# Kernel tuning notes

Hardware: AMD Instinct MI355X
Metric: run time of the kernel (lower is better)

## Reference

```python
import jax, jax.numpy as jnp
import numpy as np

B, T, C = 2, 2048, 1024
H, DK, DV = 16, 64, 64


def setup_inputs() -> dict:
    key = jax.random.key(0)
    ks = jax.random.split(key, 12)
    p = lambda k, shape: (jax.random.normal(k, shape, dtype=jnp.float32) * 0.02)
    Q = jax.random.normal(ks[0], (B, T, C), dtype=jnp.float32)
    K = jax.random.normal(ks[1], (B, T, C), dtype=jnp.float32)
    V = jax.random.normal(ks[2], (B, T, C), dtype=jnp.float32)
    Wq, bq = p(ks[3], (C, H * DK)), p(ks[4], (H * DK,))
    Wk, bk = p(ks[5], (C, H * DK)), p(ks[6], (H * DK,))
    Wv, bv = p(ks[7], (C, H * DV)), p(ks[8], (H * DV,))
    Wo, bo = p(ks[9], (H * DV, C)), p(ks[10], (C,))
    # additive causal mask, broadcastable to (B, H, T, T)
    causal = jnp.tril(jnp.ones((T, T), dtype=bool))
    mask = jnp.where(causal, 0.0, -1e9).astype(jnp.float32)[None, None]
    return {"Q": Q, "K": K, "V": V, "Wq": Wq, "bq": bq, "Wk": Wk, "bk": bk,
            "Wv": Wv, "bv": bv, "Wo": Wo, "bo": bo, "mask": mask}


def reference(Q, K, V, Wq, bq, Wk, bk, Wv, bv, Wo, bo, mask):
    def split(x, d):  # (B,T,H*d) -> (B,H,T,d)
        return x.reshape(B, T, H, d).transpose(0, 2, 1, 3)

    q = split(Q @ Wq + bq, DK)
    k = split(K @ Wk + bk, DK)
    v = split(V @ Wv + bv, DV)
    # NOTE: faithful to source — mask added BEFORE scaling by 1/sqrt(dk)
    scores = (jnp.einsum('bhqd,bhkd->bhqk', q, k) + mask) / float(np.sqrt(DK))
    attn = jax.nn.softmax(scores, axis=-1)
    out = jnp.einsum('bhqk,bhkd->bhqd', attn, v)  # (B,H,T,DV)
    out = out.transpose(0, 2, 1, 3).reshape(B, T, H * DV)
    return out @ Wo + bo
```

## Files before the change

kernel.cpp:

```cpp
#include <hip/hip_runtime.h>
#include <cstdint>
#include <cstddef>

#define TB 2
#define TT 2048
#define TC 1024
#define TH 16
#define TD 64
#define MROWS (TB*TT)

typedef __attribute__((ext_vector_type(8))) short bf16x8;
typedef __attribute__((ext_vector_type(4))) float f32x4;

#define QSCL2 0.18033688011112042f
#define MASKL2 (-1.8033688e8f)

__device__ __forceinline__ unsigned short f2bf(float f) {
  union { float f; unsigned int u; } x; x.f = f;
  unsigned int r = x.u + 0x7fffu + ((x.u >> 16) & 1u);
  return (unsigned short)(r >> 16);
}

__device__ __forceinline__ void gload16(const void* g, void* l) {
  __builtin_amdgcn_global_load_lds((const __attribute__((address_space(1))) void*)g,
                                   (__attribute__((address_space(3))) void*)l, 16, 0, 0);
}

#define WAITVM(N) do { asm volatile("s_waitcnt vmcnt(" #N ")" ::: "memory"); \
                       __builtin_amdgcn_sched_barrier(0); } while (0)

__device__ __forceinline__ float exp2h(float x) {
  float r;
  asm("v_exp_f32 %0, %1" : "=v"(r) : "v"(x));
  return r;
}

__global__ __launch_bounds__(256) void prep_kernel(
    const float* __restrict__ W0, const float* __restrict__ W1,
    const float* __restrict__ W2, const float* __restrict__ W3,
    unsigned short* __restrict__ T0, unsigned short* __restrict__ T1,
    unsigned short* __restrict__ T2, unsigned short* __restrict__ T3,
    const float* __restrict__ Q, const float* __restrict__ K, const float* __restrict__ V,
    unsigned short* __restrict__ qc, unsigned short* __restrict__ kc,
    unsigned short* __restrict__ vc) {
  const int z = blockIdx.z;
  if (z < 4) {
    const float* W = z == 0 ? W0 : (z == 1 ? W1 : (z == 2 ? W2 : W3));
    unsigned short* WT = z == 0 ? T0 : (z == 1 ? T1 : (z == 2 ? T2 : T3));
    __shared__ float ts[32][33];
    int tx = threadIdx.x & 31, ty = threadIdx.x >> 5;
    int n0 = blockIdx.x * 32, k0 = blockIdx.y * 32;
#pragma unroll
    for (int r = 0; r < 32; r += 8)
      ts[ty + r][tx] = W[(size_t)(k0 + ty + r) * TC + n0 + tx];
    __syncthreads();
#pragma unroll
    for (int r = 0; r < 32; r += 8)
      WT[(size_t)(n0 + ty + r) * TC + k0 + tx] = f2bf(ts[tx][ty + r]);
  } else {
    const int zt = z - 4;
    const float* in = zt == 0 ? Q : (zt == 1 ? K : V);
    unsigned short* out = zt == 0 ? qc : (zt == 1 ? kc : vc);
    const int lb = blockIdx.y * 32 + blockIdx.x;
#pragma unroll
    for (int c = 0; c < 2; ++c) {
      int i = lb * 4096 + c * 2048 + threadIdx.x * 8;
      float4 f0 = *(const float4*)(in + i);
      float4 f1 = *(const float4*)(in + i + 4);
      union { unsigned short u[8]; int4 v; } pk;
      pk.u[0] = f2bf(f0.x); pk.u[1] = f2bf(f0.y); pk.u[2] = f2bf(f0.z); pk.u[3] = f2bf(f0.w);
      pk.u[4] = f2bf(f1.x); pk.u[5] = f2bf(f1.y); pk.u[6] = f2bf(f1.z); pk.u[7] = f2bf(f1.w);
      *(int4*)(out + i) = pk.v;
    }
  }
}

__global__ __launch_bounds__(256) void wtrans4_kernel(
    const float* __restrict__ W0, const float* __restrict__ W1,
    const float* __restrict__ W2, const float* __restrict__ W3,
    unsigned short* __restrict__ T0, unsigned short* __restrict__ T1,
    unsigned short* __restrict__ T2, unsigned short* __restrict__ T3) {
  const int z = blockIdx.z;
  const float* W = z == 0 ? W0 : (z == 1 ? W1 : (z == 2 ? W2 : W3));
  unsigned short* WT = z == 0 ? T0 : (z == 1 ? T1 : (z == 2 ? T2 : T3));
  __shared__ float ts[32][33];
  int tx = threadIdx.x & 31, ty = threadIdx.x >> 5;
  int n0 = blockIdx.x * 32, k0 = blockIdx.y * 32;
#pragma unroll
  for (int r = 0; r < 32; r += 8)
    ts[ty + r][tx] = W[(size_t)(k0 + ty + r) * TC + n0 + tx];
  __syncthreads();
#pragma unroll
  for (int r = 0; r < 32; r += 8)
    WT[(size_t)(n0 + ty + r) * TC + k0 + tx] = f2bf(ts[tx][ty + r]);
}

__global__ __launch_bounds__(256) void cast3_kernel(
    const float* __restrict__ A, const float* __restrict__ B, const float* __restrict__ C,
    unsigned short* __restrict__ oa, unsigned short* __restrict__ ob,
    unsigned short* __restrict__ oc) {
  const int z = blockIdx.y;
  const float* in = z == 0 ? A : (z == 1 ? B : C);
  unsigned short* out = z == 0 ? oa : (z == 1 ? ob : oc);
  int i = (blockIdx.x * 256 + threadIdx.x) * 8;
  float4 f0 = *(const float4*)(in + i);
  float4 f1 = *(const float4*)(in + i + 4);
  union { unsigned short u[8]; int4 v; } pk;
  pk.u[0] = f2bf(f0.x); pk.u[1] = f2bf(f0.y); pk.u[2] = f2bf(f0.z); pk.u[3] = f2bf(f0.w);
  pk.u[4] = f2bf(f1.x); pk.u[5] = f2bf(f1.y); pk.u[6] = f2bf(f1.z); pk.u[7] = f2bf(f1.w);
  *(int4*)(out + i) = pk.v;
}

__global__ __launch_bounds__(256, 6)
void qkv_gemm_kernel(const unsigned short* __restrict__ Aq, const unsigned short* __restrict__ Ak,
                     const unsigned short* __restrict__ Av,
                     const unsigned short* __restrict__ BTq, const unsigned short* __restrict__ BTk,
                     const unsigned short* __restrict__ BTv,
                     const float* __restrict__ bq, const float* __restrict__ bk,
                     const float* __restrict__ bv,
                     unsigned short* __restrict__ Oq, unsigned short* __restrict__ Ok,
                     unsigned short* __restrict__ Ov, int zbase) {
  __shared__ __attribute__((aligned(16))) unsigned short As[128][64];
  __shared__ __attribute__((aligned(16))) unsigned short Bs[64][64];
  const int z = blockIdx.z + zbase;
  const unsigned short* A  = z == 0 ? Aq  : (z == 1 ? Ak  : Av);
  const unsigned short* Bt = z == 0 ? BTq : (z == 1 ? BTk : BTv);
  const float* bias        = z == 0 ? bq  : (z == 1 ? bk  : bv);
  unsigned short* Out      = z == 0 ? Oq  : (z == 1 ? Ok  : Ov);

  const int lin = blockIdx.y * 16 + blockIdx.x;
  const int swz = (lin & 7) * 64 + (lin >> 3);
  const int m0 = (swz >> 4) * 128, n0 = (swz & 15) * 64;

  const int tid = threadIdx.x, wave = tid >> 6, lane = tid & 63;
  const int lh = lane & 15, lq = lane >> 4;
  const int wr = wave >> 1, wc = wave & 1;
  const int srow = lane >> 3, sseg = (lane & 7) ^ srow;
  const f32x4 vzero = {0.f, 0.f, 0.f, 0.f};
  f32x4 acc[4][2];
#pragma unroll
  for (int i = 0; i < 4; ++i)
#pragma unroll
    for (int j = 0; j < 2; ++j) acc[i][j] = vzero;

  for (int k0 = 0; k0 < TC; k0 += 64) {
    __syncthreads();
#pragma unroll
    for (int c = 0; c < 4; ++c) {
      const int chunk = wave * 4 + c;
      const int row = chunk * 8 + srow;
      gload16(A + (size_t)(m0 + row) * TC + k0 + sseg * 8, &As[chunk * 8][0]);
    }
#pragma unroll
    for (int c = 0; c < 2; ++c) {
      const int chunk = wave * 2 + c;
      const int row = chunk * 8 + srow;
      gload16(Bt + (size_t)(n0 + row) * TC + k0 + sseg * 8, &Bs[chunk * 8][0]);
    }
    __syncthreads();
#pragma unroll
    for (int kk = 0; kk < 2; ++kk) {
      const int seg = kk * 4 + lq;
      bf16x8 a[4], b[2];
#pragma unroll
      for (int i = 0; i < 4; ++i) {
        int row = wr * 64 + i * 16 + lh;
        a[i] = *(const bf16x8*)&As[row][(seg ^ (row & 7)) << 3];
      }
#pragma unroll
      for (int j = 0; j < 2; ++j) {
        int row = wc * 32 + j * 16 + lh;
        b[j] = *(const bf16x8*)&Bs[row][(seg ^ (row & 7)) << 3];
      }
#pragma unroll
      for (int i = 0; i < 4; ++i)
#pragma unroll
        for (int j = 0; j < 2; ++j)
          acc[i][j] = __builtin_amdgcn_mfma_f32_16x16x32_bf16(a[i], b[j], acc[i][j], 0, 0, 0);
    }
  }

#pragma unroll
  for (int i = 0; i < 4; ++i)
#pragma unroll
    for (int j = 0; j < 2; ++j) {
      const int cg = n0 + wc * 32 + j * 16 + lh;
      const float bb = bias[cg];
      if (z == 2) {
        int rg0 = m0 + wr * 64 + i * 16 + lq * 4;
        int bidx = rg0 >> 11, t0 = rg0 & (TT - 1);
        int h = cg >> 6, d = cg & 63;
        unsigned long long pk = 0ull;
#pragma unroll
        for (int r = 0; r < 4; ++r)
          pk |= (unsigned long long)f2bf(acc[i][j][r] + bb) << (16 * r);
        *(unsigned long long*)(Out + ((size_t)((bidx * TH + h) * TD + d)) * TT + t0) = pk;
      } else {
#pragma unroll
        for (int r = 0; r < 4; ++r) {
          int rg = m0 + wr * 64 + i * 16 + lq * 4 + r;
          int bidx = rg >> 11, t = rg & (TT - 1);
          int h = cg >> 6, d = cg & 63;
          Out[((size_t)((bidx * TH + h) * TT + t)) * TD + d] = f2bf(acc[i][j][r] + bb);
        }
      }
    }
}

__global__ __launch_bounds__(256, 4)
void oproj_gemm_kernel(const unsigned short* __restrict__ A, const unsigned short* __restrict__ Bt,
                       const float* __restrict__ bias, float* __restrict__ Out) {
  __shared__ __attribute__((aligned(16))) unsigned short As[64][64];
  __shared__ __attribute__((aligned(16))) unsigned short Bs[64][64];
  const int lin = blockIdx.y * 16 + blockIdx.x;
  const int swz = (lin & 7) * 128 + (lin >> 3);
  const int m0 = (swz >> 4) * 64, n0 = (swz & 15) * 64;

  const int tid = threadIdx.x, wave = tid >> 6, lane = tid & 63;
  const int lh = lane & 15, lq = lane >> 4;
  const int wr = wave >> 1, wc = wave & 1;
  const int srow = lane >> 3, sseg = (lane & 7) ^ srow;
  const f32x4 vzero = {0.f, 0.f, 0.f, 0.f};
  f32x4 acc[2][2];
#pragma unroll
  for (int i = 0; i < 2; ++i)
#pragma unroll
    for (int j = 0; j < 2; ++j) acc[i][j] = vzero;

  for (int k0 = 0; k0 < TC; k0 += 64) {
    __syncthreads();
#pragma unroll
    for (int c = 0; c < 2; ++c) {
      const int chunk = wave * 2 + c;
      const int row = chunk * 8 + srow;
      gload16(A + (size_t)(m0 + row) * TC + k0 + sseg * 8, &As[chunk * 8][0]);
      gload16(Bt + (size_t)(n0 + row) * TC + k0 + sseg * 8, &Bs[chunk * 8][0]);
    }
    __syncthreads();
#pragma unroll
    for (int kk = 0; kk < 2; ++kk) {
      const int seg = kk * 4 + lq;
      bf16x8 a[2], b[2];
#pragma unroll
      for (int i = 0; i < 2; ++i) {
        int row = wr * 32 + i * 16 + lh;
        a[i] = *(const bf16x8*)&As[row][(seg ^ (row & 7)) << 3];
      }
#pragma unroll
      for (int j = 0; j < 2; ++j) {
        int row = wc * 32 + j * 16 + lh;
        b[j] = *(const bf16x8*)&Bs[row][(seg ^ (row & 7)) << 3];
      }
#pragma unroll
      for (int i = 0; i < 2; ++i)
#pragma unroll
        for (int j = 0; j < 2; ++j)
          acc[i][j] = __builtin_amdgcn_mfma_f32_16x16x32_bf16(a[i], b[j], acc[i][j], 0, 0, 0);
    }
  }

#pragma unroll
  for (int i = 0; i < 2; ++i)
#pragma unroll
    for (int j = 0; j < 2; ++j) {
      const int cg = n0 + wc * 32 + j * 16 + lh;
      const float bb = bias[cg];
#pragma unroll
      for (int r = 0; r < 4; ++r) {
        int rg = m0 + wr * 32 + i * 16 + lq * 4 + r;
        Out[(size_t)rg * TC + cg] = acc[i][j][r] + bb;
      }
    }
}

__global__ __launch_bounds__(256, 4)
void attn_kernel(const unsigned short* __restrict__ qb, const unsigned short* __restrict__ kb,
                 const unsigned short* __restrict__ vtb, unsigned short* __restrict__ ob) {
  __shared__ __attribute__((aligned(16))) unsigned short Qs[64][64];
  __shared__ __attribute__((aligned(16))) unsigned short Ks[2][64][64];
  __shared__ __attribute__((aligned(16))) unsigned short Vs[2][64][64];
  const int tid = threadIdx.x, wave = tid >> 6, lane = tid & 63;
  const int lh = lane & 15, lq = lane >> 4;
  const int srow = lane >> 3, sseg = (lane & 7) ^ srow;
  const int swzA = lh & 7;

  const int id = blockIdx.x;
  const int bh = (id & 7) * 4 + ((id >> 3) & 3);
  const int bx = 31 - (id >> 5);
  const size_t qkb = (size_t)bh * TT * TD;
  const size_t vob = (size_t)bh * TD * TT;
  const int bidx = bh >> 4, h = bh & 15;
  const f32x4 vzero = {0.f, 0.f, 0.f, 0.f};

  union { unsigned short u[8]; bf16x8 v; } onef;
#pragma unroll
  for (int i = 0; i < 8; ++i) onef.u[i] = 0x3F80;

  auto stageKV = [&](int buf, int t) {
    const int kv0 = t * 64;
#pragma unroll
    for (int c = 0; c < 2; ++c) {
      const int chunk = wave * 2 + c;
      const int row = chunk * 8 + srow;
      gload16(kb + qkb + (size_t)(kv0 + row) * TD + sseg * 8, &Ks[buf][chunk * 8][0]);
      gload16(vtb + vob + (size_t)row * TT + kv0 + sseg * 8, &Vs[buf][chunk * 8][0]);
    }
  };

  const int q0 = bx * 64;
  const int nt = bx + 1;
  const int q_g = q0 + wave * 16 + lh;

#pragma unroll
  for (int c = 0; c < 2; ++c) {
    const int chunk = wave * 2 + c;
    const int row = chunk * 8 + srow;
    gload16(qb + qkb + (size_t)(q0 + row) * TD + sseg * 8, &Qs[chunk * 8][0]);
  }
  stageKV(0, 0);
  WAITVM(0);
  bf16x8 aq[2];
  {
    const int row = wave * 16 + lh;
#pragma unroll
    for (int kk = 0; kk < 2; ++kk)
      aq[kk] = *(const bf16x8*)&Qs[row][((kk * 4 + lq) ^ (row & 7)) << 3];
  }
  f32x4 oacc[4], lacc = vzero;
#pragma unroll
  for (int jt = 0; jt < 4; ++jt) oacc[jt] = vzero;

  for (int t = 0; t < nt; ++t) {
    const int cur = t & 1;
    const int kv0 = t * 64;
    __builtin_amdgcn_s_barrier();
    if (t + 1 < nt) stageKV(cur ^ 1, t + 1);

    f32x4 accS[4];
#pragma unroll
    for (int j = 0; j < 4; ++j) accS[j] = vzero;
    __builtin_amdgcn_s_setprio(1);
#pragma unroll
    for (int kk = 0; kk < 2; ++kk) {
#pragma unroll
      for (int j = 0; j < 4; ++j) {
        bf16x8 bk = *(const bf16x8*)&Ks[cur][j * 16 + lh][((kk * 4 + lq) ^ swzA) << 3];
        accS[j] = __builtin_amdgcn_mfma_f32_16x16x32_bf16(bk, aq[kk], accS[j], 0, 0, 0);
      }
    }
    __builtin_amdgcn_s_setprio(0);

    float p_[16];
    if (t == bx) {
#pragma unroll
      for (int j = 0; j < 4; ++j)
#pragma unroll
        for (int r = 0; r < 4; ++r) {
          const int kvg = kv0 + j * 16 + lq * 4 + r;
          p_[j * 4 + r] = fmaf(accS[j][r], QSCL2, (kvg <= q_g) ? 0.f : MASKL2);
        }
    } else {
#pragma unroll
      for (int j = 0; j < 4; ++j)
#pragma unroll
        for (int r = 0; r < 4; ++r)
          p_[j * 4 + r] = accS[j][r] * QSCL2;
    }
#pragma unroll
    for (int i = 0; i < 16; ++i) p_[i] = exp2h(p_[i]);

    unsigned Dw[8];
#pragma unroll
    for (int j = 0; j < 4; ++j)
#pragma unroll
      for (int tt = 0; tt < 2; ++tt)
        asm("v_cvt_pk_bf16_f32 %0, %1, %2"
            : "=v"(Dw[j * 2 + tt]) : "v"(p_[j * 4 + 2 * tt]), "v"(p_[j * 4 + 2 * tt + 1]));
#pragma unroll
    for (int ks = 0; ks < 2; ++ks) {
      unsigned x0 = Dw[(2 * ks) * 2 + 0], y0 = Dw[(2 * ks + 1) * 2 + 0];
      unsigned x1 = Dw[(2 * ks) * 2 + 1], y1 = Dw[(2 * ks + 1) * 2 + 1];
      asm("v_permlane32_swap_b32 %0, %1" : "+v"(x0), "+v"(y0));
      asm("v_permlane16_swap_b32 %0, %1" : "+v"(x0), "+v"(y0));
      asm("v_permlane32_swap_b32 %0, %1" : "+v"(x1), "+v"(y1));
      asm("v_permlane16_swap_b32 %0, %1" : "+v"(x1), "+v"(y1));
      union { unsigned u[4]; bf16x8 v; } pb;
      pb.u[0] = x0; pb.u[1] = x1; pb.u[2] = y0; pb.u[3] = y1;
      __builtin_amdgcn_s_setprio(1);
#pragma unroll
      for (int jt = 0; jt < 4; ++jt) {
        bf16x8 av = *(const bf16x8*)&Vs[cur][jt * 16 + lh][((ks * 4 + lq) ^ swzA) << 3];
        oacc[jt] = __builtin_amdgcn_mfma_f32_16x16x32_bf16(av, pb.v, oacc[jt], 0, 0, 0);
      }
      lacc = __builtin_amdgcn_mfma_f32_16x16x32_bf16(onef.v, pb.v, lacc, 0, 0, 0);
      __builtin_amdgcn_s_setprio(0);
    }
    if (t + 1 < nt) WAITVM(0);
  }

  const float inv = 1.f / lacc[0];
  unsigned short* orow = ob + ((size_t)(bidx * TT + q_g)) * TC + h * TD;
#pragma unroll
  for (int jt = 0; jt < 4; ++jt) {
    unsigned long long pk = 0ull;
#pragma unroll
    for (int r = 0; r < 4; ++r)
      pk |= (unsigned long long)f2bf(oacc[jt][r] * inv) << (16 * r);
    *(unsigned long long*)(orow + jt * 16 + lq * 4) = pk;
  }
}

extern "C" void kernel_launch(void* const* d_in, const int* in_sizes, int n_in,
                              void* d_out, int out_size, void* d_ws, size_t ws_size,
                              hipStream_t stream) {
  const float* Q  = (const float*)d_in[0];
  const float* K  = (const float*)d_in[1];
  const float* V  = (const float*)d_in[2];
  const float* Wq = (const float*)d_in[3];
  const float* bq = (const float*)d_in[4];
  const float* Wk = (const float*)d_in[5];
  const float* bk = (const float*)d_in[6];
  const float* Wv = (const float*)d_in[7];
  const float* bv = (const float*)d_in[8];
  const float* Wo = (const float*)d_in[9];
  const float* bo = (const float*)d_in[10];
  float* out = (float*)d_out;

  char* ws = (char*)d_ws;
  const size_t MB = 1ull << 20;
  unsigned short* WqT = (unsigned short*)(ws + 0 * MB);
  unsigned short* WkT = (unsigned short*)(ws + 2 * MB);
  unsigned short* WvT = (unsigned short*)(ws + 4 * MB);
  unsigned short* WoT = (unsigned short*)(ws + 6 * MB);

  const bool fat = ws_size >= 56 * MB;
  unsigned short *qc, *kc, *vc, *qbuf, *kbuf, *vtbuf, *aout;
  if (fat) {
    qc    = (unsigned short*)(ws + 8 * MB);
    kc    = (unsigned short*)(ws + 16 * MB);
    vc    = (unsigned short*)(ws + 24 * MB);
    qbuf  = (unsigned short*)(ws + 32 * MB);
    kbuf  = (unsigned short*)(ws + 40 * MB);
    vtbuf = (unsigned short*)(ws + 48 * MB);
    aout  = qc;
  } else {
    qc = kc = vc = (unsigned short*)(ws + 8 * MB);
    qbuf  = (unsigned short*)(ws + 16 * MB);
    kbuf  = (unsigned short*)(ws + 24 * MB);
    vtbuf = (unsigned short*)(ws + 32 * MB);
    aout  = qc;
  }

  dim3 blk(256);
  if (fat) {
    prep_kernel<<<dim3(32, 32, 7), blk, 0, stream>>>(
        Wq, Wk, Wv, Wo, WqT, WkT, WvT, WoT, Q, K, V, qc, kc, vc);
    qkv_gemm_kernel<<<dim3(16, 32, 3), blk, 0, stream>>>(
        qc, kc, vc, WqT, WkT, WvT, bq, bk, bv, qbuf, kbuf, vtbuf, 0);
  } else {
    const int castGrid = MROWS * TC / (256 * 8);
    wtrans4_kernel<<<dim3(32, 32, 4), blk, 0, stream>>>(Wq, Wk, Wv, Wo, WqT, WkT, WvT, WoT);
    cast3_kernel<<<dim3(castGrid, 1), blk, 0, stream>>>(Q, Q, Q, qc, qc, qc);
    qkv_gemm_kernel<<<dim3(16, 32, 1), blk, 0, stream>>>(
        qc, qc, qc, WqT, WkT, WvT, bq, bk, bv, qbuf, kbuf, vtbuf, 0);
    cast3_kernel<<<dim3(castGrid, 1), blk, 0, stream>>>(K, K, K, kc, kc, kc);
    qkv_gemm_kernel<<<dim3(16, 32, 1), blk, 0, stream>>>(
        kc, kc, kc, WqT, WkT, WvT, bq, bk, bv, qbuf, kbuf, vtbuf, 1);
    cast3_kernel<<<dim3(castGrid, 1), blk, 0, stream>>>(V, V, V, vc, vc, vc);
    qkv_gemm_kernel<<<dim3(16, 32, 1), blk, 0, stream>>>(
        vc, vc, vc, WqT, WkT, WvT, bq, bk, bv, qbuf, kbuf, vtbuf, 2);
  }

  attn_kernel<<<dim3(1024), blk, 0, stream>>>(qbuf, kbuf, vtbuf, aout);

  oproj_gemm_kernel<<<dim3(16, 64), blk, 0, stream>>>(aout, WoT, bo, out);
}
```

Before: 102.8 us.

## Fuse fp32-to-bf16 activation cast into QKV GEMM and double-buffer output projection

Removes the separate activation cast pass: the QKV GEMM now reads fp32 Q/K/V directly, converts to bf16 with packed convert instructions and stores to LDS through registers instead of direct global-to-LDS loads. This drops a full write and re-read of the bf16 activation copies and the small-workspace fallback path. The output projection GEMM gains double-buffered LDS staging so the next K tile loads while the current tile is multiplied. The trade-off is that the QKV loads now pass through VGPRs and read twice as many bytes per tile, which may expose latency in the inner loop.

```diff
diff --git a/kernel.cpp b/kernel.cpp
--- a/kernel.cpp
+++ b/kernel.cpp
@@ -35,47 +35,13 @@
   return r;
 }
 
+__device__ __forceinline__ unsigned cvtpk(float lo, float hi) {
+  unsigned r;
+  asm("v_cvt_pk_bf16_f32 %0, %1, %2" : "=v"(r) : "v"(lo), "v"(hi));
+  return r;
+}
+
 __global__ __launch_bounds__(256) void prep_kernel(
-    const float* __restrict__ W0, const float* __restrict__ W1,
-    const float* __restrict__ W2, const float* __restrict__ W3,
-    unsigned short* __restrict__ T0, unsigned short* __restrict__ T1,
-    unsigned short* __restrict__ T2, unsigned short* __restrict__ T3,
-    const float* __restrict__ Q, const float* __restrict__ K, const float* __restrict__ V,
-    unsigned short* __restrict__ qc, unsigned short* __restrict__ kc,
-    unsigned short* __restrict__ vc) {
-  const int z = blockIdx.z;
-  if (z < 4) {
-    const float* W = z == 0 ? W0 : (z == 1 ? W1 : (z == 2 ? W2 : W3));
-    unsigned short* WT = z == 0 ? T0 : (z == 1 ? T1 : (z == 2 ? T2 : T3));
-    __shared__ float ts[32][33];
-    int tx = threadIdx.x & 31, ty = threadIdx.x >> 5;
-    int n0 = blockIdx.x * 32, k0 = blockIdx.y * 32;
-#pragma unroll
-    for (int r = 0; r < 32; r += 8)
-      ts[ty + r][tx] = W[(size_t)(k0 + ty + r) * TC + n0 + tx];
-    __syncthreads();
-#pragma unroll
-    for (int r = 0; r < 32; r += 8)
-      WT[(size_t)(n0 + ty + r) * TC + k0 + tx] = f2bf(ts[tx][ty + r]);
-  } else {
-    const int zt = z - 4;
-    const float* in = zt == 0 ? Q : (zt == 1 ? K : V);
-    unsigned short* out = zt == 0 ? qc : (zt == 1 ? kc : vc);
-    const int lb = blockIdx.y * 32 + blockIdx.x;
-#pragma unroll
-    for (int c = 0; c < 2; ++c) {
-      int i = lb * 4096 + c * 2048 + threadIdx.x * 8;
-      float4 f0 = *(const float4*)(in + i);
-      float4 f1 = *(const float4*)(in + i + 4);
-      union { unsigned short u[8]; int4 v; } pk;
-      pk.u[0] = f2bf(f0.x); pk.u[1] = f2bf(f0.y); pk.u[2] = f2bf(f0.z); pk.u[3] = f2bf(f0.w);
-      pk.u[4] = f2bf(f1.x); pk.u[5] = f2bf(f1.y); pk.u[6] = f2bf(f1.z); pk.u[7] = f2bf(f1.w);
-      *(int4*)(out + i) = pk.v;
-    }
-  }
-}
-
-__global__ __launch_bounds__(256) void wtrans4_kernel(
     const float* __restrict__ W0, const float* __restrict__ W1,
     const float* __restrict__ W2, const float* __restrict__ W3,
     unsigned short* __restrict__ T0, unsigned short* __restrict__ T1,
@@ -95,35 +61,19 @@
     WT[(size_t)(n0 + ty + r) * TC + k0 + tx] = f2bf(ts[tx][ty + r]);
 }
 
-__global__ __launch_bounds__(256) void cast3_kernel(
-    const float* __restrict__ A, const float* __restrict__ B, const float* __restrict__ C,
-    unsigned short* __restrict__ oa, unsigned short* __restrict__ ob,
-    unsigned short* __restrict__ oc) {
-  const int z = blockIdx.y;
-  const float* in = z == 0 ? A : (z == 1 ? B : C);
-  unsigned short* out = z == 0 ? oa : (z == 1 ? ob : oc);
-  int i = (blockIdx.x * 256 + threadIdx.x) * 8;
-  float4 f0 = *(const float4*)(in + i);
-  float4 f1 = *(const float4*)(in + i + 4);
-  union { unsigned short u[8]; int4 v; } pk;
-  pk.u[0] = f2bf(f0.x); pk.u[1] = f2bf(f0.y); pk.u[2] = f2bf(f0.z); pk.u[3] = f2bf(f0.w);
-  pk.u[4] = f2bf(f1.x); pk.u[5] = f2bf(f1.y); pk.u[6] = f2bf(f1.z); pk.u[7] = f2bf(f1.w);
-  *(int4*)(out + i) = pk.v;
-}
-
 __global__ __launch_bounds__(256, 6)
-void qkv_gemm_kernel(const unsigned short* __restrict__ Aq, const unsigned short* __restrict__ Ak,
-                     const unsigned short* __restrict__ Av,
+void qkv_gemm_kernel(const float* __restrict__ Aq, const float* __restrict__ Ak,
+                     const float* __restrict__ Av,
                      const unsigned short* __restrict__ BTq, const unsigned short* __restrict__ BTk,
                      const unsigned short* __restrict__ BTv,
                      const float* __restrict__ bq, const float* __restrict__ bk,
                      const float* __restrict__ bv,
                      unsigned short* __restrict__ Oq, unsigned short* __restrict__ Ok,
-                     unsigned short* __restrict__ Ov, int zbase) {
+                     unsigned short* __restrict__ Ov) {
   __shared__ __attribute__((aligned(16))) unsigned short As[128][64];
   __shared__ __attribute__((aligned(16))) unsigned short Bs[64][64];
-  const int z = blockIdx.z + zbase;
-  const unsigned short* A  = z == 0 ? Aq  : (z == 1 ? Ak  : Av);
+  const int z = blockIdx.z;
+  const float* A           = z == 0 ? Aq  : (z == 1 ? Ak  : Av);
   const unsigned short* Bt = z == 0 ? BTq : (z == 1 ? BTk : BTv);
   const float* bias        = z == 0 ? bq  : (z == 1 ? bk  : bv);
   unsigned short* Out      = z == 0 ? Oq  : (z == 1 ? Ok  : Ov);
@@ -136,6 +86,7 @@
   const int lh = lane & 15, lq = lane >> 4;
   const int wr = wave >> 1, wc = wave & 1;
   const int srow = lane >> 3, sseg = (lane & 7) ^ srow;
+  const int lcol = (lane & 7) * 8;
   const f32x4 vzero = {0.f, 0.f, 0.f, 0.f};
   f32x4 acc[4][2];
 #pragma unroll
@@ -147,9 +98,14 @@
     __syncthreads();
 #pragma unroll
     for (int c = 0; c < 4; ++c) {
-      const int chunk = wave * 4 + c;
-      const int row = chunk * 8 + srow;
-      gload16(A + (size_t)(m0 + row) * TC + k0 + sseg * 8, &As[chunk * 8][0]);
+      const int row = (wave * 4 + c) * 8 + srow;
+      const float* g = A + (size_t)(m0 + row) * TC + k0 + sseg * 8;
+      float4 f0 = *(const float4*)g;
+      float4 f1 = *(const float4*)(g + 4);
+      union { unsigned u[4]; int4 v; } pk;
+      pk.u[0] = cvtpk(f0.x, f0.y); pk.u[1] = cvtpk(f0.z, f0.w);
+      pk.u[2] = cvtpk(f1.x, f1.y); pk.u[3] = cvtpk(f1.z, f1.w);
+      *(int4*)&As[row][lcol] = pk.v;
     }
 #pragma unroll
     for (int c = 0; c < 2; ++c) {
@@ -210,8 +166,8 @@
 __global__ __launch_bounds__(256, 4)
 void oproj_gemm_kernel(const unsigned short* __restrict__ A, const unsigned short* __restrict__ Bt,
                        const float* __restrict__ bias, float* __restrict__ Out) {
-  __shared__ __attribute__((aligned(16))) unsigned short As[64][64];
-  __shared__ __attribute__((aligned(16))) unsigned short Bs[64][64];
+  __shared__ __attribute__((aligned(16))) unsigned short As[2][64][64];
+  __shared__ __attribute__((aligned(16))) unsigned short Bs[2][64][64];
   const int lin = blockIdx.y * 16 + blockIdx.x;
   const int swz = (lin & 7) * 128 + (lin >> 3);
   const int m0 = (swz >> 4) * 64, n0 = (swz & 15) * 64;
@@ -227,16 +183,22 @@
 #pragma unroll
     for (int j = 0; j < 2; ++j) acc[i][j] = vzero;
 
-  for (int k0 = 0; k0 < TC; k0 += 64) {
-    __syncthreads();
+  auto stage = [&](int buf, int k0) {
 #pragma unroll
     for (int c = 0; c < 2; ++c) {
       const int chunk = wave * 2 + c;
       const int row = chunk * 8 + srow;
-      gload16(A + (size_t)(m0 + row) * TC + k0 + sseg * 8, &As[chunk * 8][0]);
-      gload16(Bt + (size_t)(n0 + row) * TC + k0 + sseg * 8, &Bs[chunk * 8][0]);
-    }
-    __syncthreads();
+      gload16(A + (size_t)(m0 + row) * TC + k0 + sseg * 8, &As[buf][chunk * 8][0]);
+      gload16(Bt + (size_t)(n0 + row) * TC + k0 + sseg * 8, &Bs[buf][chunk * 8][0]);
+    }
+  };
+
+  stage(0, 0);
+  WAITVM(0);
+  for (int kt = 0; kt < 16; ++kt) {
+    const int cur = kt & 1;
+    __builtin_amdgcn_s_barrier();
+    if (kt + 1 < 16) stage(cur ^ 1, (kt + 1) * 64);
 #pragma unroll
     for (int kk = 0; kk < 2; ++kk) {
       const int seg = kk * 4 + lq;
@@ -244,12 +206,12 @@
 #pragma unroll
       for (int i = 0; i < 2; ++i) {
         int row = wr * 32 + i * 16 + lh;
-        a[i] = *(const bf16x8*)&As[row][(seg ^ (row & 7)) << 3];
+        a[i] = *(const bf16x8*)&As[cur][row][(seg ^ (row & 7)) << 3];
       }
 #pragma unroll
       for (int j = 0; j < 2; ++j) {
         int row = wc * 32 + j * 16 + lh;
-        b[j] = *(const bf16x8*)&Bs[row][(seg ^ (row & 7)) << 3];
+        b[j] = *(const bf16x8*)&Bs[cur][row][(seg ^ (row & 7)) << 3];
       }
 #pragma unroll
       for (int i = 0; i < 2; ++i)
@@ -257,6 +219,7 @@
         for (int j = 0; j < 2; ++j)
           acc[i][j] = __builtin_amdgcn_mfma_f32_16x16x32_bf16(a[i], b[j], acc[i][j], 0, 0, 0);
     }
+    if (kt + 1 < 16) WAITVM(0);
   }
 
 #pragma unroll
@@ -374,8 +337,7 @@
     for (int j = 0; j < 4; ++j)
 #pragma unroll
       for (int tt = 0; tt < 2; ++tt)
-        asm("v_cvt_pk_bf16_f32 %0, %1, %2"
-            : "=v"(Dw[j * 2 + tt]) : "v"(p_[j * 4 + 2 * tt]), "v"(p_[j * 4 + 2 * tt + 1]));
+        Dw[j * 2 + tt] = cvtpk(p_[j * 4 + 2 * tt], p_[j * 4 + 2 * tt + 1]);
 #pragma unroll
     for (int ks = 0; ks < 2; ++ks) {
       unsigned x0 = Dw[(2 * ks) * 2 + 0], y0 = Dw[(2 * ks + 1) * 2 + 0];
@@ -432,44 +394,16 @@
   unsigned short* WkT = (unsigned short*)(ws + 2 * MB);
   unsigned short* WvT = (unsigned short*)(ws + 4 * MB);
   unsigned short* WoT = (unsigned short*)(ws + 6 * MB);
-
-  const bool fat = ws_size >= 56 * MB;
-  unsigned short *qc, *kc, *vc, *qbuf, *kbuf, *vtbuf, *aout;
-  if (fat) {
-    qc    = (unsigned short*)(ws + 8 * MB);
-    kc    = (unsigned short*)(ws + 16 * MB);
-    vc    = (unsigned short*)(ws + 24 * MB);
-    qbuf  = (unsigned short*)(ws + 32 * MB);
-    kbuf  = (unsigned short*)(ws + 40 * MB);
-    vtbuf = (unsigned short*)(ws + 48 * MB);
-    aout  = qc;
-  } else {
-    qc = kc = vc = (unsigned short*)(ws + 8 * MB);
-    qbuf  = (unsigned short*)(ws + 16 * MB);
-    kbuf  = (unsigned short*)(ws + 24 * MB);
-    vtbuf = (unsigned short*)(ws + 32 * MB);
-    aout  = qc;
-  }
+  unsigned short* aout  = (unsigned short*)(ws + 8 * MB);
+  unsigned short* qbuf  = (unsigned short*)(ws + 16 * MB);
+  unsigned short* kbuf  = (unsigned short*)(ws + 24 * MB);
+  unsigned short* vtbuf = (unsigned short*)(ws + 32 * MB);
 
   dim3 blk(256);
-  if (fat) {
-    prep_kernel<<<dim3(32, 32, 7), blk, 0, stream>>>(
-        Wq, Wk, Wv, Wo, WqT, WkT, WvT, WoT, Q, K, V, qc, kc, vc);
-    qkv_gemm_kernel<<<dim3(16, 32, 3), blk, 0, stream>>>(
-        qc, kc, vc, WqT, WkT, WvT, bq, bk, bv, qbuf, kbuf, vtbuf, 0);
-  } else {
-    const int castGrid = MROWS * TC / (256 * 8);
-    wtrans4_kernel<<<dim3(32, 32, 4), blk, 0, stream>>>(Wq, Wk, Wv, Wo, WqT, WkT, WvT, WoT);
-    cast3_kernel<<<dim3(castGrid, 1), blk, 0, stream>>>(Q, Q, Q, qc, qc, qc);
-    qkv_gemm_kernel<<<dim3(16, 32, 1), blk, 0, stream>>>(
-        qc, qc, qc, WqT, WkT, WvT, bq, bk, bv, qbuf, kbuf, vtbuf, 0);
-    cast3_kernel<<<dim3(castGrid, 1), blk, 0, stream>>>(K, K, K, kc, kc, kc);
-    qkv_gemm_kernel<<<dim3(16, 32, 1), blk, 0, stream>>>(
-        kc, kc, kc, WqT, WkT, WvT, bq, bk, bv, qbuf, kbuf, vtbuf, 1);
-    cast3_kernel<<<dim3(castGrid, 1), blk, 0, stream>>>(V, V, V, vc, vc, vc);
-    qkv_gemm_kernel<<<dim3(16, 32, 1), blk, 0, stream>>>(
-        vc, vc, vc, WqT, WkT, WvT, bq, bk, bv, qbuf, kbuf, vtbuf, 2);
-  }
+  prep_kernel<<<dim3(32, 32, 4), blk, 0, stream>>>(Wq, Wk, Wv, Wo, WqT, WkT, WvT, WoT);
+
+  qkv_gemm_kernel<<<dim3(16, 32, 3), blk, 0, stream>>>(
+      Q, K, V, WqT, WkT, WvT, bq, bk, bv, qbuf, kbuf, vtbuf);
 
   attn_kernel<<<dim3(1024), blk, 0, stream>>>(qbuf, kbuf, vtbuf, aout);
 
```

New measurement: 111.9 us. 8.8% more time.
